# Kernel optimization log

Hardware: AMD Instinct MI355X
Metric: run time of the kernel (lower is better)

## Reference

```python
import jax, jax.numpy as jnp
import numpy as np
import math

BS, S, DIM, H = 2, 2048, 1024, 16
DH = DIM // H


def setup_inputs() -> dict:
    key = jax.random.key(0)
    ks = jax.random.split(key, 11)
    std = 1.0 / math.sqrt(DIM)
    inp = {
        "query": jax.random.normal(ks[0], (BS, S, DIM), jnp.float32),
        "key_": jax.random.normal(ks[1], (BS, S, DIM), jnp.float32),
        "value": jax.random.normal(ks[2], (BS, S, DIM), jnp.float32),
        "mask": jnp.ones((BS, S), jnp.int32),
        "q_w": jax.random.normal(ks[3], (DIM, DIM), jnp.float32) * std,
        "q_b": jnp.zeros((DIM,), jnp.float32),
        "k_w": jax.random.normal(ks[4], (DIM, DIM), jnp.float32) * std,
        "k_b": jnp.zeros((DIM,), jnp.float32),
        "v_w": jax.random.normal(ks[5], (DIM, DIM), jnp.float32) * std,
        "v_b": jnp.zeros((DIM,), jnp.float32),
        "o_w": jax.random.normal(ks[6], (DIM, DIM), jnp.float32) * std,
        "o_b": jnp.zeros((DIM,), jnp.float32),
    }
    return inp


def _shape(x):
    # (bs, s, dim) -> (bs, h, s, dh)
    return x.reshape(BS, -1, H, DH).transpose(0, 2, 1, 3)


def reference(query, key_, value, mask, q_w, q_b, k_w, k_b, v_w, v_b, o_w, o_b):
    # linear projections (torch Linear: x @ W.T + b)
    q = _shape(query @ q_w.T + q_b) / math.sqrt(DH)
    k = _shape(key_ @ k_w.T + k_b)
    v = _shape(value @ v_w.T + v_b)
    # scores: (bs, h, s, s)
    scores = jnp.einsum("bhqd,bhkd->bhqk", q, k)
    pad = (mask == 0)[:, None, None, :]  # (bs,1,1,k_len)
    scores = jnp.where(pad, -jnp.inf, scores)
    weights = jax.nn.softmax(scores, axis=-1)
    context = jnp.einsum("bhqk,bhkd->bhqd", weights, v)
    context = context.transpose(0, 2, 1, 3).reshape(BS, -1, DIM)
    return context @ o_w.T + o_b
```

## Files before the change

kernel.cpp:

```cpp
#include <hip/hip_runtime.h>
#include <hip/hip_bf16.h>

#define BSZ 2
#define SEQ 2048
#define DIMN 1024
#define NH 16
#define DH 64
#define LOG2E 1.4426950408889634f

typedef unsigned short ushort_t;
typedef __attribute__((ext_vector_type(8))) short short8;
typedef __attribute__((ext_vector_type(4))) float float4v;

__device__ __forceinline__ ushort_t f2bf(float f) {
    union { float f; unsigned int u; } c; c.f = f;
    return (ushort_t)((c.u + 0x8000u) >> 16);
}
__device__ __forceinline__ unsigned int pkbf(float a, float b) {
    __hip_bfloat162 h = __float22bfloat162_rn(make_float2(a, b));
    unsigned int u; __builtin_memcpy(&u, &h, 4); return u;
}
__device__ __forceinline__ unsigned int pkbf_asm(float a, float b) {
    unsigned int d;
    asm("v_cvt_pk_bf16_f32 %0, %1, %2" : "=v"(d) : "v"(a), "v"(b));
    return d;
}
__device__ __forceinline__ float exp2_raw(float x) {
    float d; asm("v_exp_f32 %0, %1" : "=v"(d) : "v"(x)); return d;
}
__device__ __forceinline__ float max3f(float a, float b, float c) {
    float d; asm("v_max3_f32 %0, %1, %2, %3" : "=v"(d) : "v"(a), "v"(b), "v"(c)); return d;
}
__device__ __forceinline__ void gld16(const ushort_t* g, ushort_t* l) {
    __builtin_amdgcn_global_load_lds(
        (const __attribute__((address_space(1))) unsigned int*)g,
        (__attribute__((address_space(3))) unsigned int*)l, 16, 0, 0);
}

__global__ __launch_bounds__(256) void cvt_all(
    const float* __restrict__ w0, const float* __restrict__ w1,
    const float* __restrict__ w2, const float* __restrict__ w3,
    const float* __restrict__ x0, const float* __restrict__ x1,
    const float* __restrict__ x2,
    ushort_t* __restrict__ o0, ushort_t* __restrict__ o1,
    ushort_t* __restrict__ o2, ushort_t* __restrict__ o3,
    ushort_t* __restrict__ xb)
{
    const int y = blockIdx.y;
    if (y < 4) {
        const float* s; ushort_t* d;
        switch (y) {
            case 0: s = w0; d = o0; break;
            case 1: s = w1; d = o1; break;
            case 2: s = w2; d = o2; break;
            default: s = w3; d = o3; break;
        }
        int i = (blockIdx.x * 256 + threadIdx.x) * 4;
        float4v v = *(const float4v*)(s + i);
        uint2 o; o.x = pkbf(v[0], v[1]); o.y = pkbf(v[2], v[3]);
        *(uint2*)(d + i) = o;
    } else {
        const int m = y - 4;
        const float* s = (m == 0) ? x0 : (m == 1) ? x1 : x2;
        ushort_t* d = xb + (size_t)m * (BSZ * SEQ * DIMN);
        size_t base = (size_t)blockIdx.x * 4096;
#pragma unroll
        for (int j = 0; j < 4; ++j) {
            size_t i = base + j * 1024 + threadIdx.x * 4;
            float4v v = *(const float4v*)(s + i);
            uint2 o; o.x = pkbf(v[0], v[1]); o.y = pkbf(v[2], v[3]);
            *(uint2*)(d + i) = o;
        }
    }
}

__global__ __launch_bounds__(256) void gemm_qkv(
    const float* __restrict__ xq, const float* __restrict__ xk, const float* __restrict__ xv,
    const ushort_t* __restrict__ Wq, const ushort_t* __restrict__ Wk, const ushort_t* __restrict__ Wv,
    const float* __restrict__ qb, const float* __restrict__ kb, const float* __restrict__ vb,
    ushort_t* __restrict__ Qp, ushort_t* __restrict__ Kp, ushort_t* __restrict__ VpT)
{
    __shared__ ushort_t As[128 * 72];
    __shared__ ushort_t Bs[128 * 72];
    const int tid  = threadIdx.x;
    const int lane = tid & 63;
    const int w    = tid >> 6;
    const int wm   = w >> 1, wn = w & 1;
    const int quad = lane >> 4;
    const int l16  = lane & 15;
    const int mBase = blockIdx.y * 128;
    const int nGlob = blockIdx.x * 128;
    const int z     = nGlob >> 10;
    const int nBase = nGlob & 1023;
    const float*    A    = (z == 0) ? xq : (z == 1) ? xk : xv;
    const ushort_t* W    = (z == 0) ? Wq : (z == 1) ? Wk : Wv;
    const float*    bias = (z == 0) ? qb : (z == 1) ? kb : vb;

    float4v acc[4][4];
    const float4v z4 = {0.f, 0.f, 0.f, 0.f};
#pragma unroll
    for (int i = 0; i < 4; ++i)
#pragma unroll
        for (int j = 0; j < 4; ++j) acc[i][j] = z4;

    for (int k0 = 0; k0 < 1024; k0 += 64) {
        float4v a[4][2];
        short8  wb[4];
#pragma unroll
        for (int it = 0; it < 4; ++it) {
            int c = it * 256 + tid, row = c >> 3, col = (c & 7) * 8;
            const float* g = A + (size_t)(mBase + row) * 1024 + k0 + col;
            a[it][0] = *(const float4v*)g;
            a[it][1] = *(const float4v*)(g + 4);
            wb[it] = *(const short8*)(W + (size_t)(nBase + row) * 1024 + k0 + col);
        }
        __syncthreads();
#pragma unroll
        for (int it = 0; it < 4; ++it) {
            int c = it * 256 + tid, row = c >> 3, col = (c & 7) * 8;
            uint4 ua;
            ua.x = pkbf(a[it][0][0], a[it][0][1]); ua.y = pkbf(a[it][0][2], a[it][0][3]);
            ua.z = pkbf(a[it][1][0], a[it][1][1]); ua.w = pkbf(a[it][1][2], a[it][1][3]);
            *(uint4*)&As[row * 72 + col] = ua;
            *(short8*)&Bs[row * 72 + col] = wb[it];
        }
        __syncthreads();

#pragma unroll
        for (int ksub = 0; ksub < 2; ++ksub) {
            short8 af[4], bf[4];
#pragma unroll
            for (int mt = 0; mt < 4; ++mt)
                af[mt] = *(const short8*)&As[(wm * 64 + mt * 16 + l16) * 72 + ksub * 32 + quad * 8];
#pragma unroll
            for (int nt = 0; nt < 4; ++nt)
                bf[nt] = *(const short8*)&Bs[(wn * 64 + nt * 16 + l16) * 72 + ksub * 32 + quad * 8];
#pragma unroll
            for (int mt = 0; mt < 4; ++mt)
#pragma unroll
                for (int nt = 0; nt < 4; ++nt)
                    acc[mt][nt] = __builtin_amdgcn_mfma_f32_16x16x32_bf16(af[mt], bf[nt], acc[mt][nt], 0, 0, 0);
        }
    }

    const float scale = (z == 0) ? 0.125f * LOG2E : 1.0f;
    if (z < 2) {
        ushort_t* C = (z == 0) ? Qp : Kp;
#pragma unroll
        for (int mt = 0; mt < 4; ++mt)
#pragma unroll
            for (int nt = 0; nt < 4; ++nt) {
                int colg = nBase + wn * 64 + nt * 16 + l16;
                float bv = bias[colg];
#pragma unroll
                for (int r = 0; r < 4; ++r) {
                    int rowg = mBase + wm * 64 + mt * 16 + quad * 4 + r;
                    C[(size_t)rowg * 1024 + colg] = f2bf((acc[mt][nt][r] + bv) * scale);
                }
            }
    } else {
#pragma unroll
        for (int mt = 0; mt < 4; ++mt)
#pragma unroll
            for (int nt = 0; nt < 4; ++nt) {
                int n = nBase + wn * 64 + nt * 16 + l16;
                int hh = n >> 6, d = n & 63;
                float bv = bias[n];
                int rowg = mBase + wm * 64 + mt * 16 + quad * 4;
                int b = rowg >> 11, s = rowg & 2047;
                uint2 pk;
                pk.x = pkbf(acc[mt][nt][0] + bv, acc[mt][nt][1] + bv);
                pk.y = pkbf(acc[mt][nt][2] + bv, acc[mt][nt][3] + bv);
                *(uint2*)&VpT[(((size_t)(b * 16 + hh) * 64 + d) << 11) + s] = pk;
            }
    }
}

__global__ __launch_bounds__(256) void gemm_qkv_fast(
    const ushort_t* __restrict__ Xb,
    const ushort_t* __restrict__ Wq, const ushort_t* __restrict__ Wk, const ushort_t* __restrict__ Wv,
    const float* __restrict__ qb, const float* __restrict__ kb, const float* __restrict__ vb,
    ushort_t* __restrict__ Qp, ushort_t* __restrict__ Kp, ushort_t* __restrict__ VpT)
{
    __shared__ __align__(16) ushort_t As[128 * 64];
    __shared__ __align__(16) ushort_t Bs[128 * 64];
    const int tid  = threadIdx.x;
    const int lane = tid & 63;
    const int w    = tid >> 6;
    const int wm   = w >> 1, wn = w & 1;
    const int quad = lane >> 4;
    const int l16  = lane & 15;
    const int sw   = l16 & 7;
    const int mBase = blockIdx.y * 128;
    const int nGlob = blockIdx.x * 128;
    const int z     = nGlob >> 10;
    const int nBase = nGlob & 1023;
    const ushort_t* A    = Xb + (size_t)z * (BSZ * SEQ * DIMN);
    const ushort_t* W    = (z == 0) ? Wq : (z == 1) ? Wk : Wv;
    const float*    bias = (z == 0) ? qb : (z == 1) ? kb : vb;

    const int srow = tid >> 3;
    const int sc   = tid & 7;

    float4v acc[4][4];
    const float4v z4 = {0.f, 0.f, 0.f, 0.f};
#pragma unroll
    for (int i = 0; i < 4; ++i)
#pragma unroll
        for (int j = 0; j < 4; ++j) acc[i][j] = z4;

    for (int k0 = 0; k0 < 1024; k0 += 64) {
#pragma unroll
        for (int itq = 0; itq < 4; ++itq) {
            int row = itq * 32 + srow;
            int colsw = (sc ^ (row & 7)) * 8;
            gld16(A + (size_t)(mBase + row) * 1024 + k0 + colsw, &As[(itq * 32 + w * 8) * 64]);
            gld16(W + (size_t)(nBase + row) * 1024 + k0 + colsw, &Bs[(itq * 32 + w * 8) * 64]);
        }
        __syncthreads();

#pragma unroll
        for (int ksub = 0; ksub < 2; ++ksub) {
            short8 af[4], bf[4];
#pragma unroll
            for (int mt = 0; mt < 4; ++mt)
                af[mt] = *(const short8*)&As[(wm * 64 + mt * 16 + l16) * 64 + ((ksub * 4 + quad) ^ sw) * 8];
#pragma unroll
            for (int nt = 0; nt < 4; ++nt)
                bf[nt] = *(const short8*)&Bs[(wn * 64 + nt * 16 + l16) * 64 + ((ksub * 4 + quad) ^ sw) * 8];
#pragma unroll
            for (int mt = 0; mt < 4; ++mt)
#pragma unroll
                for (int nt = 0; nt < 4; ++nt)
                    acc[mt][nt] = __builtin_amdgcn_mfma_f32_16x16x32_bf16(af[mt], bf[nt], acc[mt][nt], 0, 0, 0);
        }
        __syncthreads();
    }

    const float scale = (z == 0) ? 0.125f * LOG2E : 1.0f;
    if (z < 2) {
        ushort_t* C = (z == 0) ? Qp : Kp;
#pragma unroll
        for (int mt = 0; mt < 4; ++mt)
#pragma unroll
            for (int nt = 0; nt < 4; ++nt) {
                int colg = nBase + wn * 64 + nt * 16 + l16;
                float bv = bias[colg];
#pragma unroll
                for (int r = 0; r < 4; ++r) {
                    int rowg = mBase + wm * 64 + mt * 16 + quad * 4 + r;
                    C[(size_t)rowg * 1024 + colg] = f2bf((acc[mt][nt][r] + bv) * scale);
                }
            }
    } else {
#pragma unroll
        for (int mt = 0; mt < 4; ++mt)
#pragma unroll
            for (int nt = 0; nt < 4; ++nt) {
                int n = nBase + wn * 64 + nt * 16 + l16;
                int hh = n >> 6, d = n & 63;
                float bv = bias[n];
                int rowg = mBase + wm * 64 + mt * 16 + quad * 4;
                int b = rowg >> 11, s = rowg & 2047;
                uint2 pk;
                pk.x = pkbf(acc[mt][nt][0] + bv, acc[mt][nt][1] + bv);
                pk.y = pkbf(acc[mt][nt][2] + bv, acc[mt][nt][3] + bv);
                *(uint2*)&VpT[(((size_t)(b * 16 + hh) * 64 + d) << 11) + s] = pk;
            }
    }
}

__global__ __launch_bounds__(256) void gemm_o(
    const ushort_t* __restrict__ A, const ushort_t* __restrict__ W,
    const float* __restrict__ bias, float* __restrict__ C)
{
    __shared__ __align__(16) ushort_t As[128 * 64];
    __shared__ __align__(16) ushort_t Bs[64 * 64];
    const int tid  = threadIdx.x;
    const int lane = tid & 63;
    const int w    = tid >> 6;
    const int wm   = w & 1, wn = w >> 1;
    const int quad = lane >> 4;
    const int l16  = lane & 15;
    const int sw   = l16 & 7;
    const int mBase = blockIdx.y * 128;
    const int nBase = blockIdx.x * 64;
    const int srow = tid >> 3;
    const int sc   = tid & 7;

    float4v acc[4][2];
    const float4v z4 = {0.f, 0.f, 0.f, 0.f};
#pragma unroll
    for (int mt = 0; mt < 4; ++mt)
#pragma unroll
        for (int nt = 0; nt < 2; ++nt) acc[mt][nt] = z4;

    for (int k0 = 0; k0 < 1024; k0 += 64) {
#pragma unroll
        for (int itq = 0; itq < 4; ++itq) {
            int row = itq * 32 + srow;
            gld16(A + (size_t)(mBase + row) * 1024 + k0 + ((sc ^ (row & 7)) * 8),
                  &As[(itq * 32 + w * 8) * 64]);
        }
#pragma unroll
        for (int itq = 0; itq < 2; ++itq) {
            int row = itq * 32 + srow;
            gld16(W + (size_t)(nBase + row) * 1024 + k0 + ((sc ^ (row & 7)) * 8),
                  &Bs[(itq * 32 + w * 8) * 64]);
        }
        __syncthreads();

#pragma unroll
        for (int ksub = 0; ksub < 2; ++ksub) {
            short8 af[4], bf[2];
#pragma unroll
            for (int mt = 0; mt < 4; ++mt)
                af[mt] = *(const short8*)&As[(wm * 64 + mt * 16 + l16) * 64 + ((ksub * 4 + quad) ^ sw) * 8];
#pragma unroll
            for (int nt = 0; nt < 2; ++nt)
                bf[nt] = *(const short8*)&Bs[(wn * 32 + nt * 16 + l16) * 64 + ((ksub * 4 + quad) ^ sw) * 8];
#pragma unroll
            for (int mt = 0; mt < 4; ++mt)
#pragma unroll
                for (int nt = 0; nt < 2; ++nt)
                    acc[mt][nt] = __builtin_amdgcn_mfma_f32_16x16x32_bf16(af[mt], bf[nt], acc[mt][nt], 0, 0, 0);
        }
        __syncthreads();
    }

#pragma unroll
    for (int mt = 0; mt < 4; ++mt)
#pragma unroll
        for (int nt = 0; nt < 2; ++nt) {
            int colg = nBase + wn * 32 + nt * 16 + l16;
            float bv = bias[colg];
#pragma unroll
            for (int r = 0; r < 4; ++r) {
                int rowg = mBase + wm * 64 + mt * 16 + quad * 4 + r;
                C[(size_t)rowg * 1024 + colg] = acc[mt][nt][r] + bv;
            }
        }
}

__global__ __launch_bounds__(512) void attn_kernel(
    const ushort_t* __restrict__ Qp, const ushort_t* __restrict__ Kp,
    const ushort_t* __restrict__ VpT, const int* __restrict__ mask,
    ushort_t* __restrict__ Cp)
{
    __shared__ __align__(16) ushort_t Ps[2][128 * 64];
    __shared__ __align__(16) ushort_t Ks[2][64 * 64];
    __shared__ __align__(16) ushort_t Vt[3][64 * 64];
    __shared__ int s_mok[8];

    const int tid  = threadIdx.x;
    const int lane = tid & 63;
    const int w    = tid >> 6;
    const int quad = lane >> 4;
    const int l16  = lane & 15;
    const int sw   = l16 & 7;
    const int b    = blockIdx.x >> 4;
    const int h    = blockIdx.x & 15;
    const int q0   = blockIdx.y * 128;

    const int srow = tid >> 3;
    const int sc   = tid & 7;
    const int gsc  = (sc ^ (srow & 7)) * 8;
    const ushort_t* Vbase = VpT + ((size_t)(b * 16 + h) * 64) * 2048;
    const ushort_t* Kbase = Kp + (size_t)b * SEQ * DIMN + h * DH;
    const ushort_t* Qbase = Qp + (size_t)(b * SEQ + q0) * DIMN + h * DH;

    {
        int m0 = mask[b * SEQ + tid];
        int m1 = mask[b * SEQ + 512 + tid];
        int m2 = mask[b * SEQ + 1024 + tid];
        int m3 = mask[b * SEQ + 1536 + tid];
        int ok = __all((m0 != 0) & (m1 != 0) & (m2 != 0) & (m3 != 0));
        if (lane == 0) s_mok[w] = ok;
    }

#pragma unroll
    for (int it2 = 0; it2 < 2; ++it2) {
        int row = it2 * 64 + srow;
        gld16(Qbase + (size_t)row * DIMN + ((sc ^ (row & 7)) * 8),
              &Ps[0][(it2 * 64 + w * 8) * 64]);
    }
    gld16(Kbase + (size_t)srow * DIMN + gsc, &Ks[0][w * 512]);
    gld16(Vbase + (size_t)srow * 2048 + gsc, &Vt[0][w * 512]);
    __syncthreads();

    const int mall = s_mok[0] & s_mok[1] & s_mok[2] & s_mok[3]
                   & s_mok[4] & s_mok[5] & s_mok[6] & s_mok[7];

    short8 bq[2];
#pragma unroll
    for (int ks = 0; ks < 2; ++ks)
        bq[ks] = *(const short8*)&Ps[0][(w * 16 + l16) * 64 + ((4 * ks + quad) ^ sw) * 8];

    const float4v z4 = {0.f, 0.f, 0.f, 0.f};
    float4v Oacc[4];
#pragma unroll
    for (int vt = 0; vt < 4; ++vt) Oacc[vt] = z4;
    float4v Lacc = z4;
    float mrow = 0.0f;
    float4v mneg4 = z4;

    short8 ones;
#pragma unroll
    for (int j = 0; j < 8; ++j) ones[j] = (short)0x3F80;

    const int NT = SEQ / 64;
    const int prow = (w * 16 + l16) * 64;

    {
        gld16(Kbase + (size_t)(64 + srow) * DIMN + gsc, &Ks[1][w * 512]);
        gld16(Vbase + (size_t)srow * 2048 + 64 + gsc, &Vt[1][w * 512]);

        float4v Sv[4];
        __builtin_amdgcn_s_setprio(1);
#pragma unroll
        for (int kt = 0; kt < 4; ++kt) {
            short8 ak = *(const short8*)&Ks[0][(kt * 16 + l16) * 64 + (quad ^ sw) * 8];
            Sv[kt] = __builtin_amdgcn_mfma_f32_16x16x32_bf16(ak, bq[0], mneg4, 0, 0, 0);
        }
#pragma unroll
        for (int kt = 0; kt < 4; ++kt) {
            short8 ak = *(const short8*)&Ks[0][(kt * 16 + l16) * 64 + ((4 + quad) ^ sw) * 8];
            Sv[kt] = __builtin_amdgcn_mfma_f32_16x16x32_bf16(ak, bq[1], Sv[kt], 0, 0, 0);
        }
        __builtin_amdgcn_s_setprio(0);

        if (!mall) {
#pragma unroll
            for (int kt = 0; kt < 4; ++kt) {
                int4 mv = *(const int4*)(mask + b * SEQ + kt * 16 + quad * 4);
#pragma unroll
                for (int r = 0; r < 4; ++r) {
                    int m = (r == 0) ? mv.x : (r == 1) ? mv.y : (r == 2) ? mv.z : mv.w;
                    Sv[kt][r] += (m == 0) ? -1e30f : 0.0f;
                }
            }
        }

        float a0 = max3f(Sv[0][0], Sv[0][1], Sv[0][2]);
        float a1 = max3f(Sv[0][3], Sv[1][0], Sv[1][1]);
        float a2 = max3f(Sv[1][2], Sv[1][3], Sv[2][0]);
        float a3 = max3f(Sv[2][1], Sv[2][2], Sv[2][3]);
        float a4 = max3f(Sv[3][0], Sv[3][1], Sv[3][2]);
        float b0 = max3f(a0, a1, Sv[3][3]);
        float b1 = max3f(a2, a3, a4);
        float mx = fmaxf(b0, b1);
        mx = fmaxf(mx, __shfl_xor(mx, 16));
        mx = fmaxf(mx, __shfl_xor(mx, 32));
        if (!__all(mx <= 8.0f)) {
            float d = fmaxf(mx, 0.0f);
            float alpha = exp2_raw(-d);
            mrow += d;
#pragma unroll
            for (int vt = 0; vt < 4; ++vt) Oacc[vt] *= alpha;
            Lacc *= alpha;
#pragma unroll
            for (int kt = 0; kt < 4; ++kt)
#pragma unroll
                for (int r = 0; r < 4; ++r) Sv[kt][r] -= d;
            mneg4[0] = -mrow; mneg4[1] = -mrow; mneg4[2] = -mrow; mneg4[3] = -mrow;
        }
#pragma unroll
        for (int kt = 0; kt < 4; ++kt)
#pragma unroll
            for (int r = 0; r < 4; ++r) Sv[kt][r] = exp2_raw(Sv[kt][r]);

#pragma unroll
        for (int kt = 0; kt < 4; ++kt) {
            uint2 pk;
            pk.x = pkbf_asm(Sv[kt][0], Sv[kt][1]);
            pk.y = pkbf_asm(Sv[kt][2], Sv[kt][3]);
            int chunk = (2 * kt + (quad >> 1)) ^ sw;
            *(uint2*)&Ps[0][prow + chunk * 8 + (quad & 1) * 4] = pk;
        }
        __syncthreads();
    }

    ushort_t* vRd  = Vt[0];
    ushort_t* vCur = Vt[1];
    ushort_t* vWr  = Vt[2];

#pragma unroll 2
    for (int t = 1; t < NT; ++t) {
        const int kt0 = t * 64;

        if (t + 1 < NT) {
            gld16(Kbase + (size_t)(kt0 + 64 + srow) * DIMN + gsc, &Ks[(t + 1) & 1][w * 512]);
            gld16(Vbase + (size_t)srow * 2048 + kt0 + 64 + gsc, vWr + w * 512);
        }

        float4v Sv[4];
        __builtin_amdgcn_s_setprio(1);
#pragma unroll
        for (int kt = 0; kt < 4; ++kt) {
            short8 ak = *(const short8*)&Ks[t & 1][(kt * 16 + l16) * 64 + (quad ^ sw) * 8];
            Sv[kt] = __builtin_amdgcn_mfma_f32_16x16x32_bf16(ak, bq[0], mneg4, 0, 0, 0);
        }
#pragma unroll
        for (int kt = 0; kt < 4; ++kt) {
            short8 ak = *(const short8*)&Ks[t & 1][(kt * 16 + l16) * 64 + ((4 + quad) ^ sw) * 8];
            Sv[kt] = __builtin_amdgcn_mfma_f32_16x16x32_bf16(ak, bq[1], Sv[kt], 0, 0, 0);
        }
#pragma unroll
        for (int ks = 0; ks < 2; ++ks) {
            short8 bp = *(const short8*)&Ps[(t - 1) & 1][prow + ((4 * ks + quad) ^ sw) * 8];
            Lacc = __builtin_amdgcn_mfma_f32_16x16x32_bf16(ones, bp, Lacc, 0, 0, 0);
#pragma unroll
            for (int vt = 0; vt < 4; ++vt) {
                short8 av = *(const short8*)(vRd + (vt * 16 + l16) * 64 + ((4 * ks + quad) ^ sw) * 8);
                Oacc[vt] = __builtin_amdgcn_mfma_f32_16x16x32_bf16(av, bp, Oacc[vt], 0, 0, 0);
            }
        }
        __builtin_amdgcn_s_setprio(0);

        if (!mall) {
#pragma unroll
            for (int kt = 0; kt < 4; ++kt) {
                int4 mv = *(const int4*)(mask + b * SEQ + kt0 + kt * 16 + quad * 4);
#pragma unroll
                for (int r = 0; r < 4; ++r) {
                    int m = (r == 0) ? mv.x : (r == 1) ? mv.y : (r == 2) ? mv.z : mv.w;
                    Sv[kt][r] += (m == 0) ? -1e30f : 0.0f;
                }
            }
        }

        float a0 = max3f(Sv[0][0], Sv[0][1], Sv[0][2]);
        float a1 = max3f(Sv[0][3], Sv[1][0], Sv[1][1]);
        float a2 = max3f(Sv[1][2], Sv[1][3], Sv[2][0]);
        float a3 = max3f(Sv[2][1], Sv[2][2], Sv[2][3]);
        float a4 = max3f(Sv[3][0], Sv[3][1], Sv[3][2]);
        float b0 = max3f(a0, a1, Sv[3][3]);
        float b1 = max3f(a2, a3, a4);
        float mx = fmaxf(b0, b1);
        mx = fmaxf(mx, __shfl_xor(mx, 16));
        mx = fmaxf(mx, __shfl_xor(mx, 32));
        if (!__all(mx <= 8.0f)) {
            float d = fmaxf(mx, 0.0f);
            float alpha = exp2_raw(-d);
            mrow += d;
#pragma unroll
            for (int vt = 0; vt < 4; ++vt) Oacc[vt] *= alpha;
            Lacc *= alpha;
#pragma unroll
            for (int kt = 0; kt < 4; ++kt)
#pragma unroll
                for (int r = 0; r < 4; ++r) Sv[kt][r] -= d;
            mneg4[0] = -mrow; mneg4[1] = -mrow; mneg4[2] = -mrow; mneg4[3] = -mrow;
        }
#pragma unroll
        for (int kt = 0; kt < 4; ++kt)
#pragma unroll
            for (int r = 0; r < 4; ++r) Sv[kt][r] = exp2_raw(Sv[kt][r]);

#pragma unroll
        for (int kt = 0; kt < 4; ++kt) {
            uint2 pk;
            pk.x = pkbf_asm(Sv[kt][0], Sv[kt][1]);
            pk.y = pkbf_asm(Sv[kt][2], Sv[kt][3]);
            int chunk = (2 * kt + (quad >> 1)) ^ sw;
            *(uint2*)&Ps[t & 1][prow + chunk * 8 + (quad & 1) * 4] = pk;
        }

        __syncthreads();

        ushort_t* tmp = vRd; vRd = vCur; vCur = vWr; vWr = tmp;
    }

#pragma unroll
    for (int ks = 0; ks < 2; ++ks) {
        short8 bp = *(const short8*)&Ps[(NT - 1) & 1][prow + ((4 * ks + quad) ^ sw) * 8];
        Lacc = __builtin_amdgcn_mfma_f32_16x16x32_bf16(ones, bp, Lacc, 0, 0, 0);
#pragma unroll
        for (int vt = 0; vt < 4; ++vt) {
            short8 av = *(const short8*)(vRd + (vt * 16 + l16) * 64 + ((4 * ks + quad) ^ sw) * 8);
            Oacc[vt] = __builtin_amdgcn_mfma_f32_16x16x32_bf16(av, bp, Oacc[vt], 0, 0, 0);
        }
    }

    float inv = 1.0f / Lacc[0];
    int row = q0 + w * 16 + l16;
#pragma unroll
    for (int vt = 0; vt < 4; ++vt) {
        uint2 pk;
        pk.x = pkbf_asm(Oacc[vt][0] * inv, Oacc[vt][1] * inv);
        pk.y = pkbf_asm(Oacc[vt][2] * inv, Oacc[vt][3] * inv);
        *(uint2*)&Cp[(size_t)(b * SEQ + row) * DIMN + h * DH + vt * 16 + quad * 4] = pk;
    }
}

extern "C" void kernel_launch(void* const* d_in, const int* in_sizes, int n_in,
                              void* d_out, int out_size, void* d_ws, size_t ws_size,
                              hipStream_t stream) {
    const float* x_q = (const float*)d_in[0];
    const float* x_k = (const float*)d_in[1];
    const float* x_v = (const float*)d_in[2];
    const int*   msk = (const int*)d_in[3];
    const float* q_w = (const float*)d_in[4];
    const float* q_b = (const float*)d_in[5];
    const float* k_w = (const float*)d_in[6];
    const float* k_b = (const float*)d_in[7];
    const float* v_w = (const float*)d_in[8];
    const float* v_b = (const float*)d_in[9];
    const float* o_w = (const float*)d_in[10];
    const float* o_b = (const float*)d_in[11];
    float* out = (float*)d_out;

    const size_t NEL = (size_t)BSZ * SEQ * DIMN;
    const size_t WEL = (size_t)DIMN * DIMN;
    ushort_t* Qp  = (ushort_t*)d_ws;
    ushort_t* Kp  = Qp + NEL;
    ushort_t* VpT = Kp + NEL;
    ushort_t* Wq  = VpT + NEL;
    ushort_t* Wk  = Wq + WEL;
    ushort_t* Wv  = Wk + WEL;
    ushort_t* Wo  = Wv + WEL;
    ushort_t* Xb  = Wo + WEL;
    ushort_t* Cp  = Qp;

    const bool fast = ws_size >= ((size_t)56 << 20);
    if (fast) {
        cvt_all<<<dim3(1024, 7), 256, 0, stream>>>(q_w, k_w, v_w, o_w, x_q, x_k, x_v,
                                                   Wq, Wk, Wv, Wo, Xb);
        gemm_qkv_fast<<<dim3(24, 32), 256, 0, stream>>>(Xb, Wq, Wk, Wv,
                                                        q_b, k_b, v_b, Qp, Kp, VpT);
    } else {
        cvt_all<<<dim3(1024, 4), 256, 0, stream>>>(q_w, k_w, v_w, o_w, x_q, x_k, x_v,
                                                   Wq, Wk, Wv, Wo, Xb);
        gemm_qkv<<<dim3(24, 32), 256, 0, stream>>>(x_q, x_k, x_v, Wq, Wk, Wv,
                                                   q_b, k_b, v_b, Qp, Kp, VpT);
    }
    attn_kernel<<<dim3(BSZ * NH, SEQ / 128), 512, 0, stream>>>(Qp, Kp, VpT, msk, Cp);
    gemm_o<<<dim3(16, 32), 256, 0, stream>>>(Cp, Wo, o_b, out);
}
```

Before: 225.3 us.

## Give each attention wave 32 query rows and halve waves per block

The attention block drops from 8 waves handling 16 query rows each to 4 waves handling 32 rows each. Each K and V fragment read from LDS now feeds two MFMAs, which halves LDS traffic per MFMA. The P tile becomes single-buffered, which is safe because each wave only reads and writes its own rows. The trade-off is higher register pressure and fewer resident waves per CU (about one per SIMD), which leaves less latency hiding for the global loads and the softmax work.

```diff
diff --git a/kernel.cpp b/kernel.cpp
--- a/kernel.cpp
+++ b/kernel.cpp
@@ -342,15 +342,15 @@
         }
 }
 
-__global__ __launch_bounds__(512) void attn_kernel(
+__global__ __launch_bounds__(256) void attn_kernel(
     const ushort_t* __restrict__ Qp, const ushort_t* __restrict__ Kp,
     const ushort_t* __restrict__ VpT, const int* __restrict__ mask,
     ushort_t* __restrict__ Cp)
 {
-    __shared__ __align__(16) ushort_t Ps[2][128 * 64];
+    __shared__ __align__(16) ushort_t Ps[128 * 64];
     __shared__ __align__(16) ushort_t Ks[2][64 * 64];
     __shared__ __align__(16) ushort_t Vt[3][64 * 64];
-    __shared__ int s_mok[8];
+    __shared__ int s_mok[4];
 
     const int tid  = threadIdx.x;
     const int lane = tid & 63;
@@ -362,70 +362,82 @@
     const int h    = blockIdx.x & 15;
     const int q0   = blockIdx.y * 128;
 
-    const int srow = tid >> 3;
-    const int sc   = tid & 7;
-    const int gsc  = (sc ^ (srow & 7)) * 8;
+    const int srow8 = lane >> 3;
+    const int sc    = lane & 7;
+    const int gsc   = (sc ^ srow8) * 8;
     const ushort_t* Vbase = VpT + ((size_t)(b * 16 + h) * 64) * 2048;
     const ushort_t* Kbase = Kp + (size_t)b * SEQ * DIMN + h * DH;
     const ushort_t* Qbase = Qp + (size_t)(b * SEQ + q0) * DIMN + h * DH;
 
     {
-        int m0 = mask[b * SEQ + tid];
-        int m1 = mask[b * SEQ + 512 + tid];
-        int m2 = mask[b * SEQ + 1024 + tid];
-        int m3 = mask[b * SEQ + 1536 + tid];
-        int ok = __all((m0 != 0) & (m1 != 0) & (m2 != 0) & (m3 != 0));
+        int ok = 1;
+#pragma unroll
+        for (int j = 0; j < 8; ++j) ok &= (mask[b * SEQ + j * 256 + tid] != 0);
+        ok = __all(ok);
         if (lane == 0) s_mok[w] = ok;
     }
 
 #pragma unroll
-    for (int it2 = 0; it2 < 2; ++it2) {
-        int row = it2 * 64 + srow;
-        gld16(Qbase + (size_t)row * DIMN + ((sc ^ (row & 7)) * 8),
-              &Ps[0][(it2 * 64 + w * 8) * 64]);
-    }
-    gld16(Kbase + (size_t)srow * DIMN + gsc, &Ks[0][w * 512]);
-    gld16(Vbase + (size_t)srow * 2048 + gsc, &Vt[0][w * 512]);
+    for (int r = 0; r < 4; ++r) {
+        int row = r * 32 + w * 8 + srow8;
+        gld16(Qbase + (size_t)row * DIMN + gsc, &Ps[(r * 32 + w * 8) * 64]);
+    }
+#pragma unroll
+    for (int r = 0; r < 2; ++r) {
+        int row = r * 32 + w * 8 + srow8;
+        gld16(Kbase + (size_t)row * DIMN + gsc, &Ks[0][(r * 32 + w * 8) * 64]);
+        gld16(Vbase + (size_t)row * 2048 + gsc, &Vt[0][(r * 32 + w * 8) * 64]);
+    }
     __syncthreads();
 
-    const int mall = s_mok[0] & s_mok[1] & s_mok[2] & s_mok[3]
-                   & s_mok[4] & s_mok[5] & s_mok[6] & s_mok[7];
-
-    short8 bq[2];
-#pragma unroll
-    for (int ks = 0; ks < 2; ++ks)
-        bq[ks] = *(const short8*)&Ps[0][(w * 16 + l16) * 64 + ((4 * ks + quad) ^ sw) * 8];
+    const int mall = s_mok[0] & s_mok[1] & s_mok[2] & s_mok[3];
+
+    short8 bq[2][2];
+#pragma unroll
+    for (int nt = 0; nt < 2; ++nt)
+#pragma unroll
+        for (int ks = 0; ks < 2; ++ks)
+            bq[nt][ks] = *(const short8*)&Ps[(w * 32 + nt * 16 + l16) * 64 + ((4 * ks + quad) ^ sw) * 8];
 
     const float4v z4 = {0.f, 0.f, 0.f, 0.f};
-    float4v Oacc[4];
-#pragma unroll
-    for (int vt = 0; vt < 4; ++vt) Oacc[vt] = z4;
-    float4v Lacc = z4;
-    float mrow = 0.0f;
-    float4v mneg4 = z4;
+    float4v Oacc[4][2];
+#pragma unroll
+    for (int vt = 0; vt < 4; ++vt)
+#pragma unroll
+        for (int nt = 0; nt < 2; ++nt) Oacc[vt][nt] = z4;
+    float4v Lacc[2] = {z4, z4};
+    float mrow[2] = {0.0f, 0.0f};
+    float4v mneg[2] = {z4, z4};
 
     short8 ones;
 #pragma unroll
     for (int j = 0; j < 8; ++j) ones[j] = (short)0x3F80;
 
     const int NT = SEQ / 64;
-    const int prow = (w * 16 + l16) * 64;
+    const int prow0 = (w * 32 + l16) * 64;
+    const int prow1 = (w * 32 + 16 + l16) * 64;
 
     {
-        gld16(Kbase + (size_t)(64 + srow) * DIMN + gsc, &Ks[1][w * 512]);
-        gld16(Vbase + (size_t)srow * 2048 + 64 + gsc, &Vt[1][w * 512]);
-
-        float4v Sv[4];
+#pragma unroll
+        for (int r = 0; r < 2; ++r) {
+            int row = r * 32 + w * 8 + srow8;
+            gld16(Kbase + (size_t)(64 + row) * DIMN + gsc, &Ks[1][(r * 32 + w * 8) * 64]);
+            gld16(Vbase + (size_t)row * 2048 + 64 + gsc, &Vt[1][(r * 32 + w * 8) * 64]);
+        }
+
+        float4v Sv[4][2];
         __builtin_amdgcn_s_setprio(1);
 #pragma unroll
         for (int kt = 0; kt < 4; ++kt) {
             short8 ak = *(const short8*)&Ks[0][(kt * 16 + l16) * 64 + (quad ^ sw) * 8];
-            Sv[kt] = __builtin_amdgcn_mfma_f32_16x16x32_bf16(ak, bq[0], mneg4, 0, 0, 0);
+            Sv[kt][0] = __builtin_amdgcn_mfma_f32_16x16x32_bf16(ak, bq[0][0], mneg[0], 0, 0, 0);
+            Sv[kt][1] = __builtin_amdgcn_mfma_f32_16x16x32_bf16(ak, bq[1][0], mneg[1], 0, 0, 0);
         }
 #pragma unroll
         for (int kt = 0; kt < 4; ++kt) {
             short8 ak = *(const short8*)&Ks[0][(kt * 16 + l16) * 64 + ((4 + quad) ^ sw) * 8];
-            Sv[kt] = __builtin_amdgcn_mfma_f32_16x16x32_bf16(ak, bq[1], Sv[kt], 0, 0, 0);
+            Sv[kt][0] = __builtin_amdgcn_mfma_f32_16x16x32_bf16(ak, bq[0][1], Sv[kt][0], 0, 0, 0);
+            Sv[kt][1] = __builtin_amdgcn_mfma_f32_16x16x32_bf16(ak, bq[1][1], Sv[kt][1], 0, 0, 0);
         }
         __builtin_amdgcn_s_setprio(0);
 
@@ -436,46 +448,59 @@
 #pragma unroll
                 for (int r = 0; r < 4; ++r) {
                     int m = (r == 0) ? mv.x : (r == 1) ? mv.y : (r == 2) ? mv.z : mv.w;
-                    Sv[kt][r] += (m == 0) ? -1e30f : 0.0f;
+                    float add = (m == 0) ? -1e30f : 0.0f;
+                    Sv[kt][0][r] += add;
+                    Sv[kt][1][r] += add;
                 }
             }
         }
 
-        float a0 = max3f(Sv[0][0], Sv[0][1], Sv[0][2]);
-        float a1 = max3f(Sv[0][3], Sv[1][0], Sv[1][1]);
-        float a2 = max3f(Sv[1][2], Sv[1][3], Sv[2][0]);
-        float a3 = max3f(Sv[2][1], Sv[2][2], Sv[2][3]);
-        float a4 = max3f(Sv[3][0], Sv[3][1], Sv[3][2]);
-        float b0 = max3f(a0, a1, Sv[3][3]);
-        float b1 = max3f(a2, a3, a4);
-        float mx = fmaxf(b0, b1);
-        mx = fmaxf(mx, __shfl_xor(mx, 16));
-        mx = fmaxf(mx, __shfl_xor(mx, 32));
-        if (!__all(mx <= 8.0f)) {
-            float d = fmaxf(mx, 0.0f);
-            float alpha = exp2_raw(-d);
-            mrow += d;
-#pragma unroll
-            for (int vt = 0; vt < 4; ++vt) Oacc[vt] *= alpha;
-            Lacc *= alpha;
-#pragma unroll
-            for (int kt = 0; kt < 4; ++kt)
-#pragma unroll
-                for (int r = 0; r < 4; ++r) Sv[kt][r] -= d;
-            mneg4[0] = -mrow; mneg4[1] = -mrow; mneg4[2] = -mrow; mneg4[3] = -mrow;
+        float mx[2];
+#pragma unroll
+        for (int nt = 0; nt < 2; ++nt) {
+            float a0 = max3f(Sv[0][nt][0], Sv[0][nt][1], Sv[0][nt][2]);
+            float a1 = max3f(Sv[0][nt][3], Sv[1][nt][0], Sv[1][nt][1]);
+            float a2 = max3f(Sv[1][nt][2], Sv[1][nt][3], Sv[2][nt][0]);
+            float a3 = max3f(Sv[2][nt][1], Sv[2][nt][2], Sv[2][nt][3]);
+            float a4 = max3f(Sv[3][nt][0], Sv[3][nt][1], Sv[3][nt][2]);
+            mx[nt] = fmaxf(max3f(a0, a1, Sv[3][nt][3]), max3f(a2, a3, a4));
+        }
+        if (!__all(fmaxf(mx[0], mx[1]) <= 8.0f)) {
+#pragma unroll
+            for (int nt = 0; nt < 2; ++nt) {
+                float m2 = fmaxf(mx[nt], __shfl_xor(mx[nt], 16));
+                m2 = fmaxf(m2, __shfl_xor(m2, 32));
+                float d = fmaxf(m2, 0.0f);
+                float alpha = exp2_raw(-d);
+                mrow[nt] += d;
+#pragma unroll
+                for (int vt = 0; vt < 4; ++vt) Oacc[vt][nt] *= alpha;
+                Lacc[nt] *= alpha;
+#pragma unroll
+                for (int kt = 0; kt < 4; ++kt)
+#pragma unroll
+                    for (int r = 0; r < 4; ++r) Sv[kt][nt][r] -= d;
+                mneg[nt][0] = -mrow[nt]; mneg[nt][1] = -mrow[nt];
+                mneg[nt][2] = -mrow[nt]; mneg[nt][3] = -mrow[nt];
+            }
         }
 #pragma unroll
         for (int kt = 0; kt < 4; ++kt)
 #pragma unroll
-            for (int r = 0; r < 4; ++r) Sv[kt][r] = exp2_raw(Sv[kt][r]);
+            for (int nt = 0; nt < 2; ++nt)
+#pragma unroll
+                for (int r = 0; r < 4; ++r) Sv[kt][nt][r] = exp2_raw(Sv[kt][nt][r]);
 
 #pragma unroll
         for (int kt = 0; kt < 4; ++kt) {
-            uint2 pk;
-            pk.x = pkbf_asm(Sv[kt][0], Sv[kt][1]);
-            pk.y = pkbf_asm(Sv[kt][2], Sv[kt][3]);
-            int chunk = (2 * kt + (quad >> 1)) ^ sw;
-            *(uint2*)&Ps[0][prow + chunk * 8 + (quad & 1) * 4] = pk;
+            int chunk = ((2 * kt + (quad >> 1)) ^ sw) * 8 + (quad & 1) * 4;
+            uint2 pk0, pk1;
+            pk0.x = pkbf_asm(Sv[kt][0][0], Sv[kt][0][1]);
+            pk0.y = pkbf_asm(Sv[kt][0][2], Sv[kt][0][3]);
+            pk1.x = pkbf_asm(Sv[kt][1][0], Sv[kt][1][1]);
+            pk1.y = pkbf_asm(Sv[kt][1][2], Sv[kt][1][3]);
+            *(uint2*)&Ps[prow0 + chunk] = pk0;
+            *(uint2*)&Ps[prow1 + chunk] = pk1;
         }
         __syncthreads();
     }
@@ -489,30 +514,39 @@
         const int kt0 = t * 64;
 
         if (t + 1 < NT) {
-            gld16(Kbase + (size_t)(kt0 + 64 + srow) * DIMN + gsc, &Ks[(t + 1) & 1][w * 512]);
-            gld16(Vbase + (size_t)srow * 2048 + kt0 + 64 + gsc, vWr + w * 512);
-        }
-
-        float4v Sv[4];
+#pragma unroll
+            for (int r = 0; r < 2; ++r) {
+                int row = r * 32 + w * 8 + srow8;
+                gld16(Kbase + (size_t)(kt0 + 64 + row) * DIMN + gsc, &Ks[(t + 1) & 1][(r * 32 + w * 8) * 64]);
+                gld16(Vbase + (size_t)row * 2048 + kt0 + 64 + gsc, vWr + (r * 32 + w * 8) * 64);
+            }
+        }
+
+        float4v Sv[4][2];
         __builtin_amdgcn_s_setprio(1);
 #pragma unroll
         for (int kt = 0; kt < 4; ++kt) {
             short8 ak = *(const short8*)&Ks[t & 1][(kt * 16 + l16) * 64 + (quad ^ sw) * 8];
-            Sv[kt] = __builtin_amdgcn_mfma_f32_16x16x32_bf16(ak, bq[0], mneg4, 0, 0, 0);
+            Sv[kt][0] = __builtin_amdgcn_mfma_f32_16x16x32_bf16(ak, bq[0][0], mneg[0], 0, 0, 0);
+            Sv[kt][1] = __builtin_amdgcn_mfma_f32_16x16x32_bf16(ak, bq[1][0], mneg[1], 0, 0, 0);
         }
 #pragma unroll
         for (int kt = 0; kt < 4; ++kt) {
             short8 ak = *(const short8*)&Ks[t & 1][(kt * 16 + l16) * 64 + ((4 + quad) ^ sw) * 8];
-            Sv[kt] = __builtin_amdgcn_mfma_f32_16x16x32_bf16(ak, bq[1], Sv[kt], 0, 0, 0);
+            Sv[kt][0] = __builtin_amdgcn_mfma_f32_16x16x32_bf16(ak, bq[0][1], Sv[kt][0], 0, 0, 0);
+            Sv[kt][1] = __builtin_amdgcn_mfma_f32_16x16x32_bf16(ak, bq[1][1], Sv[kt][1], 0, 0, 0);
         }
 #pragma unroll
         for (int ks = 0; ks < 2; ++ks) {
-            short8 bp = *(const short8*)&Ps[(t - 1) & 1][prow + ((4 * ks + quad) ^ sw) * 8];
-            Lacc = __builtin_amdgcn_mfma_f32_16x16x32_bf16(ones, bp, Lacc, 0, 0, 0);
+            short8 bp0 = *(const short8*)&Ps[prow0 + ((4 * ks + quad) ^ sw) * 8];
+            short8 bp1 = *(const short8*)&Ps[prow1 + ((4 * ks + quad) ^ sw) * 8];
+            Lacc[0] = __builtin_amdgcn_mfma_f32_16x16x32_bf16(ones, bp0, Lacc[0], 0, 0, 0);
+            Lacc[1] = __builtin_amdgcn_mfma_f32_16x16x32_bf16(ones, bp1, Lacc[1], 0, 0, 0);
 #pragma unroll
             for (int vt = 0; vt < 4; ++vt) {
                 short8 av = *(const short8*)(vRd + (vt * 16 + l16) * 64 + ((4 * ks + quad) ^ sw) * 8);
-                Oacc[vt] = __builtin_amdgcn_mfma_f32_16x16x32_bf16(av, bp, Oacc[vt], 0, 0, 0);
+                Oacc[vt][0] = __builtin_amdgcn_mfma_f32_16x16x32_bf16(av, bp0, Oacc[vt][0], 0, 0, 0);
+                Oacc[vt][1] = __builtin_amdgcn_mfma_f32_16x16x32_bf16(av, bp1, Oacc[vt][1], 0, 0, 0);
             }
         }
         __builtin_amdgcn_s_setprio(0);
@@ -524,46 +558,59 @@
 #pragma unroll
                 for (int r = 0; r < 4; ++r) {
                     int m = (r == 0) ? mv.x : (r == 1) ? mv.y : (r == 2) ? mv.z : mv.w;
-                    Sv[kt][r] += (m == 0) ? -1e30f : 0.0f;
+                    float add = (m == 0) ? -1e30f : 0.0f;
+                    Sv[kt][0][r] += add;
+                    Sv[kt][1][r] += add;
                 }
             }
         }
 
-        float a0 = max3f(Sv[0][0], Sv[0][1], Sv[0][2]);
-        float a1 = max3f(Sv[0][3], Sv[1][0], Sv[1][1]);
-        float a2 = max3f(Sv[1][2], Sv[1][3], Sv[2][0]);
-        float a3 = max3f(Sv[2][1], Sv[2][2], Sv[2][3]);
-        float a4 = max3f(Sv[3][0], Sv[3][1], Sv[3][2]);
-        float b0 = max3f(a0, a1, Sv[3][3]);
-        float b1 = max3f(a2, a3, a4);
-        float mx = fmaxf(b0, b1);
-        mx = fmaxf(mx, __shfl_xor(mx, 16));
-        mx = fmaxf(mx, __shfl_xor(mx, 32));
-        if (!__all(mx <= 8.0f)) {
-            float d = fmaxf(mx, 0.0f);
-            float alpha = exp2_raw(-d);
-            mrow += d;
-#pragma unroll
-            for (int vt = 0; vt < 4; ++vt) Oacc[vt] *= alpha;
-            Lacc *= alpha;
-#pragma unroll
-            for (int kt = 0; kt < 4; ++kt)
-#pragma unroll
-                for (int r = 0; r < 4; ++r) Sv[kt][r] -= d;
-            mneg4[0] = -mrow; mneg4[1] = -mrow; mneg4[2] = -mrow; mneg4[3] = -mrow;
+        float mx[2];
+#pragma unroll
+        for (int nt = 0; nt < 2; ++nt) {
+            float a0 = max3f(Sv[0][nt][0], Sv[0][nt][1], Sv[0][nt][2]);
+            float a1 = max3f(Sv[0][nt][3], Sv[1][nt][0], Sv[1][nt][1]);
+            float a2 = max3f(Sv[1][nt][2], Sv[1][nt][3], Sv[2][nt][0]);
+            float a3 = max3f(Sv[2][nt][1], Sv[2][nt][2], Sv[2][nt][3]);
+            float a4 = max3f(Sv[3][nt][0], Sv[3][nt][1], Sv[3][nt][2]);
+            mx[nt] = fmaxf(max3f(a0, a1, Sv[3][nt][3]), max3f(a2, a3, a4));
+        }
+        if (!__all(fmaxf(mx[0], mx[1]) <= 8.0f)) {
+#pragma unroll
+            for (int nt = 0; nt < 2; ++nt) {
+                float m2 = fmaxf(mx[nt], __shfl_xor(mx[nt], 16));
+                m2 = fmaxf(m2, __shfl_xor(m2, 32));
+                float d = fmaxf(m2, 0.0f);
+                float alpha = exp2_raw(-d);
+                mrow[nt] += d;
+#pragma unroll
+                for (int vt = 0; vt < 4; ++vt) Oacc[vt][nt] *= alpha;
+                Lacc[nt] *= alpha;
+#pragma unroll
+                for (int kt = 0; kt < 4; ++kt)
+#pragma unroll
+                    for (int r = 0; r < 4; ++r) Sv[kt][nt][r] -= d;
+                mneg[nt][0] = -mrow[nt]; mneg[nt][1] = -mrow[nt];
+                mneg[nt][2] = -mrow[nt]; mneg[nt][3] = -mrow[nt];
+            }
         }
 #pragma unroll
         for (int kt = 0; kt < 4; ++kt)
 #pragma unroll
-            for (int r = 0; r < 4; ++r) Sv[kt][r] = exp2_raw(Sv[kt][r]);
+            for (int nt = 0; nt < 2; ++nt)
+#pragma unroll
+                for (int r = 0; r < 4; ++r) Sv[kt][nt][r] = exp2_raw(Sv[kt][nt][r]);
 
 #pragma unroll
         for (int kt = 0; kt < 4; ++kt) {
-            uint2 pk;
-            pk.x = pkbf_asm(Sv[kt][0], Sv[kt][1]);
-            pk.y = pkbf_asm(Sv[kt][2], Sv[kt][3]);
-            int chunk = (2 * kt + (quad >> 1)) ^ sw;
-            *(uint2*)&Ps[t & 1][prow + chunk * 8 + (quad & 1) * 4] = pk;
+            int chunk = ((2 * kt + (quad >> 1)) ^ sw) * 8 + (quad & 1) * 4;
+            uint2 pk0, pk1;
+            pk0.x = pkbf_asm(Sv[kt][0][0], Sv[kt][0][1]);
+            pk0.y = pkbf_asm(Sv[kt][0][2], Sv[kt][0][3]);
+            pk1.x = pkbf_asm(Sv[kt][1][0], Sv[kt][1][1]);
+            pk1.y = pkbf_asm(Sv[kt][1][2], Sv[kt][1][3]);
+            *(uint2*)&Ps[prow0 + chunk] = pk0;
+            *(uint2*)&Ps[prow1 + chunk] = pk1;
         }
 
         __syncthreads();
@@ -573,23 +620,29 @@
 
 #pragma unroll
     for (int ks = 0; ks < 2; ++ks) {
-        short8 bp = *(const short8*)&Ps[(NT - 1) & 1][prow + ((4 * ks + quad) ^ sw) * 8];
-        Lacc = __builtin_amdgcn_mfma_f32_16x16x32_bf16(ones, bp, Lacc, 0, 0, 0);
+        short8 bp0 = *(const short8*)&Ps[prow0 + ((4 * ks + quad) ^ sw) * 8];
+        short8 bp1 = *(const short8*)&Ps[prow1 + ((4 * ks + quad) ^ sw) * 8];
+        Lacc[0] = __builtin_amdgcn_mfma_f32_16x16x32_bf16(ones, bp0, Lacc[0], 0, 0, 0);
+        Lacc[1] = __builtin_amdgcn_mfma_f32_16x16x32_bf16(ones, bp1, Lacc[1], 0, 0, 0);
 #pragma unroll
         for (int vt = 0; vt < 4; ++vt) {
             short8 av = *(const short8*)(vRd + (vt * 16 + l16) * 64 + ((4 * ks + quad) ^ sw) * 8);
-            Oacc[vt] = __builtin_amdgcn_mfma_f32_16x16x32_bf16(av, bp, Oacc[vt], 0, 0, 0);
-        }
-    }
-
-    float inv = 1.0f / Lacc[0];
-    int row = q0 + w * 16 + l16;
-#pragma unroll
-    for (int vt = 0; vt < 4; ++vt) {
-        uint2 pk;
-        pk.x = pkbf_asm(Oacc[vt][0] * inv, Oacc[vt][1] * inv);
-        pk.y = pkbf_asm(Oacc[vt][2] * inv, Oacc[vt][3] * inv);
-        *(uint2*)&Cp[(size_t)(b * SEQ + row) * DIMN + h * DH + vt * 16 + quad * 4] = pk;
+            Oacc[vt][0] = __builtin_amdgcn_mfma_f32_16x16x32_bf16(av, bp0, Oacc[vt][0], 0, 0, 0);
+            Oacc[vt][1] = __builtin_amdgcn_mfma_f32_16x16x32_bf16(av, bp1, Oacc[vt][1], 0, 0, 0);
+        }
+    }
+
+#pragma unroll
+    for (int nt = 0; nt < 2; ++nt) {
+        float inv = 1.0f / Lacc[nt][0];
+        int row = q0 + w * 32 + nt * 16 + l16;
+#pragma unroll
+        for (int vt = 0; vt < 4; ++vt) {
+            uint2 pk;
+            pk.x = pkbf_asm(Oacc[vt][nt][0] * inv, Oacc[vt][nt][1] * inv);
+            pk.y = pkbf_asm(Oacc[vt][nt][2] * inv, Oacc[vt][nt][3] * inv);
+            *(uint2*)&Cp[(size_t)(b * SEQ + row) * DIMN + h * DH + vt * 16 + quad * 4] = pk;
+        }
     }
 }
 
@@ -634,6 +687,6 @@
         gemm_qkv<<<dim3(24, 32), 256, 0, stream>>>(x_q, x_k, x_v, Wq, Wk, Wv,
                                                    q_b, k_b, v_b, Qp, Kp, VpT);
     }
-    attn_kernel<<<dim3(BSZ * NH, SEQ / 128), 512, 0, stream>>>(Qp, Kp, VpT, msk, Cp);
+    attn_kernel<<<dim3(BSZ * NH, SEQ / 128), 256, 0, stream>>>(Qp, Kp, VpT, msk, Cp);
     gemm_o<<<dim3(16, 32), 256, 0, stream>>>(Cp, Wo, o_b, out);
 }
```

Result: no change. 229.3 us (+1.8%).

## Double-buffer LDS tiles in QKV and output projection GEMMs

Applied to the files above, without the earlier changes.

Both projection GEMM kernels now use two LDS buffers per operand. The next K-tile is issued into the alternate buffer while MFMAs run on the current one, so global load latency overlaps with compute. This doubles shared memory per block, which may reduce occupancy. Correctness depends on the existing end-of-iteration barrier ordering the buffer reuse.

```diff
diff --git a/kernel.cpp b/kernel.cpp
--- a/kernel.cpp
+++ b/kernel.cpp
@@ -182,8 +182,8 @@
     const float* __restrict__ qb, const float* __restrict__ kb, const float* __restrict__ vb,
     ushort_t* __restrict__ Qp, ushort_t* __restrict__ Kp, ushort_t* __restrict__ VpT)
 {
-    __shared__ __align__(16) ushort_t As[128 * 64];
-    __shared__ __align__(16) ushort_t Bs[128 * 64];
+    __shared__ __align__(16) ushort_t As[2][128 * 64];
+    __shared__ __align__(16) ushort_t Bs[2][128 * 64];
     const int tid  = threadIdx.x;
     const int lane = tid & 63;
     const int w    = tid >> 6;
@@ -209,25 +209,38 @@
 #pragma unroll
         for (int j = 0; j < 4; ++j) acc[i][j] = z4;
 
-    for (int k0 = 0; k0 < 1024; k0 += 64) {
-#pragma unroll
-        for (int itq = 0; itq < 4; ++itq) {
-            int row = itq * 32 + srow;
-            int colsw = (sc ^ (row & 7)) * 8;
-            gld16(A + (size_t)(mBase + row) * 1024 + k0 + colsw, &As[(itq * 32 + w * 8) * 64]);
-            gld16(W + (size_t)(nBase + row) * 1024 + k0 + colsw, &Bs[(itq * 32 + w * 8) * 64]);
-        }
-        __syncthreads();
+#pragma unroll
+    for (int itq = 0; itq < 4; ++itq) {
+        int row = itq * 32 + srow;
+        int colsw = (sc ^ (row & 7)) * 8;
+        gld16(A + (size_t)(mBase + row) * 1024 + colsw, &As[0][(itq * 32 + w * 8) * 64]);
+        gld16(W + (size_t)(nBase + row) * 1024 + colsw, &Bs[0][(itq * 32 + w * 8) * 64]);
+    }
+    __syncthreads();
+
+#pragma unroll 2
+    for (int ki = 0; ki < 16; ++ki) {
+        const int cur = ki & 1;
+        if (ki + 1 < 16) {
+            int k0n = (ki + 1) * 64;
+#pragma unroll
+            for (int itq = 0; itq < 4; ++itq) {
+                int row = itq * 32 + srow;
+                int colsw = (sc ^ (row & 7)) * 8;
+                gld16(A + (size_t)(mBase + row) * 1024 + k0n + colsw, &As[cur ^ 1][(itq * 32 + w * 8) * 64]);
+                gld16(W + (size_t)(nBase + row) * 1024 + k0n + colsw, &Bs[cur ^ 1][(itq * 32 + w * 8) * 64]);
+            }
+        }
 
 #pragma unroll
         for (int ksub = 0; ksub < 2; ++ksub) {
             short8 af[4], bf[4];
 #pragma unroll
             for (int mt = 0; mt < 4; ++mt)
-                af[mt] = *(const short8*)&As[(wm * 64 + mt * 16 + l16) * 64 + ((ksub * 4 + quad) ^ sw) * 8];
+                af[mt] = *(const short8*)&As[cur][(wm * 64 + mt * 16 + l16) * 64 + ((ksub * 4 + quad) ^ sw) * 8];
 #pragma unroll
             for (int nt = 0; nt < 4; ++nt)
-                bf[nt] = *(const short8*)&Bs[(wn * 64 + nt * 16 + l16) * 64 + ((ksub * 4 + quad) ^ sw) * 8];
+                bf[nt] = *(const short8*)&Bs[cur][(wn * 64 + nt * 16 + l16) * 64 + ((ksub * 4 + quad) ^ sw) * 8];
 #pragma unroll
             for (int mt = 0; mt < 4; ++mt)
 #pragma unroll
@@ -274,8 +287,8 @@
     const ushort_t* __restrict__ A, const ushort_t* __restrict__ W,
     const float* __restrict__ bias, float* __restrict__ C)
 {
-    __shared__ __align__(16) ushort_t As[128 * 64];
-    __shared__ __align__(16) ushort_t Bs[64 * 64];
+    __shared__ __align__(16) ushort_t As[2][128 * 64];
+    __shared__ __align__(16) ushort_t Bs[2][64 * 64];
     const int tid  = threadIdx.x;
     const int lane = tid & 63;
     const int w    = tid >> 6;
@@ -295,30 +308,44 @@
 #pragma unroll
         for (int nt = 0; nt < 2; ++nt) acc[mt][nt] = z4;
 
-    for (int k0 = 0; k0 < 1024; k0 += 64) {
-#pragma unroll
-        for (int itq = 0; itq < 4; ++itq) {
-            int row = itq * 32 + srow;
-            gld16(A + (size_t)(mBase + row) * 1024 + k0 + ((sc ^ (row & 7)) * 8),
-                  &As[(itq * 32 + w * 8) * 64]);
-        }
-#pragma unroll
-        for (int itq = 0; itq < 2; ++itq) {
-            int row = itq * 32 + srow;
-            gld16(W + (size_t)(nBase + row) * 1024 + k0 + ((sc ^ (row & 7)) * 8),
-                  &Bs[(itq * 32 + w * 8) * 64]);
-        }
-        __syncthreads();
+#pragma unroll
+    for (int itq = 0; itq < 4; ++itq) {
+        int row = itq * 32 + srow;
+        gld16(A + (size_t)(mBase + row) * 1024 + ((sc ^ (row & 7)) * 8), &As[0][(itq * 32 + w * 8) * 64]);
+    }
+#pragma unroll
+    for (int itq = 0; itq < 2; ++itq) {
+        int row = itq * 32 + srow;
+        gld16(W + (size_t)(nBase + row) * 1024 + ((sc ^ (row & 7)) * 8), &Bs[0][(itq * 32 + w * 8) * 64]);
+    }
+    __syncthreads();
+
+#pragma unroll 2
+    for (int ki = 0; ki < 16; ++ki) {
+        const int cur = ki & 1;
+        if (ki + 1 < 16) {
+            int k0n = (ki + 1) * 64;
+#pragma unroll
+            for (int itq = 0; itq < 4; ++itq) {
+                int row = itq * 32 + srow;
+                gld16(A + (size_t)(mBase + row) * 1024 + k0n + ((sc ^ (row & 7)) * 8), &As[cur ^ 1][(itq * 32 + w * 8) * 64]);
+            }
+#pragma unroll
+            for (int itq = 0; itq < 2; ++itq) {
+                int row = itq * 32 + srow;
+                gld16(W + (size_t)(nBase + row) * 1024 + k0n + ((sc ^ (row & 7)) * 8), &Bs[cur ^ 1][(itq * 32 + w * 8) * 64]);
+            }
+        }
 
 #pragma unroll
         for (int ksub = 0; ksub < 2; ++ksub) {
             short8 af[4], bf[2];
 #pragma unroll
             for (int mt = 0; mt < 4; ++mt)
-                af[mt] = *(const short8*)&As[(wm * 64 + mt * 16 + l16) * 64 + ((ksub * 4 + quad) ^ sw) * 8];
+                af[mt] = *(const short8*)&As[cur][(wm * 64 + mt * 16 + l16) * 64 + ((ksub * 4 + quad) ^ sw) * 8];
 #pragma unroll
             for (int nt = 0; nt < 2; ++nt)
-                bf[nt] = *(const short8*)&Bs[(wn * 32 + nt * 16 + l16) * 64 + ((ksub * 4 + quad) ^ sw) * 8];
+                bf[nt] = *(const short8*)&Bs[cur][(wn * 32 + nt * 16 + l16) * 64 + ((ksub * 4 + quad) ^ sw) * 8];
 #pragma unroll
             for (int mt = 0; mt < 4; ++mt)
 #pragma unroll
```

Result: no change. 228.9 us (+1.6%).
